# Optimization experiments

Measured on AMD Instinct MI355X. Metric: run time of the kernel, lower is better.

The kernel has to match this reference:

```python
import jax, jax.numpy as jnp
import numpy as np

B, L, M, C = 32, 688, 4, 32  # batch, otsl_sequence_length (= layout_prompt_length), max targets per box, tag vocab


def setup_inputs() -> dict:
    key = jax.random.key(0)
    ks = jax.random.split(key, 8)
    tag_logits = jax.random.normal(ks[0], (B, L, C), jnp.float32)
    pointer_logits = jax.random.normal(ks[1], (B, L, L), jnp.float32)
    empty_pointer_logits = jax.random.normal(ks[2], (B, 1, L), jnp.float32)
    tag_targets = jax.random.randint(ks[3], (B, L), 0, C)
    box = jax.random.randint(ks[4], (B, L, M), 0, L)
    keep = jax.random.bernoulli(ks[5], 0.5, (B, L, M))
    box_indices = jnp.where(keep, box, -1)  # -1 = padded / invalid target
    data_tag_mask = jax.random.bernoulli(ks[6], 0.3, (B, 2 * L))
    attention_mask = jax.random.bernoulli(ks[7], 0.8, (B, 2 * L)) | data_tag_mask
    return {
        'tag_logits': tag_logits,
        'pointer_logits': pointer_logits,
        'empty_pointer_logits': empty_pointer_logits,
        'tag_targets': tag_targets,
        'box_indices': box_indices,
        'data_tag_mask': data_tag_mask,
        'attention_mask': attention_mask,
    }


def reference(tag_logits, pointer_logits, empty_pointer_logits,
              tag_targets, box_indices, data_tag_mask, attention_mask):
    Bq, Lq, Cq = tag_logits.shape

    # ---- tag (cls) loss: mean cross-entropy over B*S positions ----
    logp = jax.nn.log_softmax(tag_logits, axis=-1)
    cls_loss = -jnp.mean(jnp.take_along_axis(logp, tag_targets[..., None], axis=-1))

    # ---- pointer loss: masked softmax over sequence positions ----
    seq_mask = data_tag_mask[:, Lq:]                                  # (B, L)
    mx = jnp.max(pointer_logits, axis=-1, keepdims=True)              # unmasked max, as in torch code
    exp_l = jnp.exp(pointer_logits - mx)                              # (B, L, L)
    denom = jnp.sum(exp_l * seq_mask[:, None, :], axis=-1, keepdims=True) + 1e-10
    # scatter target_mask[b, i, box_indices[b, i, m]] = True for valid entries
    valid = box_indices != -1                                         # (B, L, M)
    tgt = jnp.clip(box_indices, 0, Lq - 1)
    b_ix = jnp.arange(Bq)[:, None, None]
    r_ix = jnp.arange(Lq)[None, :, None]
    target_mask = jnp.zeros((Bq, Lq, Lq), bool).at[b_ix, r_ix, tgt].max(valid)
    losses = -jnp.log(exp_l / denom + 1e-10)                          # (B, L, L)
    masked = losses * (target_mask & seq_mask[:, None, :])
    cnt = jnp.sum(masked != 0)
    ptr_loss = jnp.where(cnt == 0, 0.0, jnp.sum(masked) / jnp.maximum(cnt, 1))

    # ---- empty pointer loss: BCE-with-logits, mean over attended positions ----
    seq2 = attention_mask[:, Lq:]                                     # (B, L)
    data2 = data_tag_mask[:, Lq:]
    targets = (seq2 & ~data2).astype(jnp.float32)
    x = empty_pointer_logits[:, 0, :]                                 # (B, L)
    bce = jnp.maximum(x, 0.0) - x * targets + jnp.log1p(jnp.exp(-jnp.abs(x)))
    vm = seq2.astype(jnp.float32)
    empty_ptr_loss = jnp.sum(bce * vm) / jnp.maximum(jnp.sum(vm), 1.0)

    # forward() returns early: total = cls + ptr + empty (no lambdas, contrastive dead code)
    total = cls_loss + ptr_loss + empty_ptr_loss
    return total, cls_loss, ptr_loss, empty_ptr_loss
```

## Files before the change

### kernel.cpp

```cpp
#include <hip/hip_runtime.h>
#include <hip/hip_bf16.h>
#include <math.h>

#define BB 32
#define LL 688
#define MM 4
#define CC 32
#define ROWS (BB * LL)
#define RPW 4
#define WPB 4
#define RPB (RPW * WPB)
#define NBLK (ROWS / RPB)

struct Partial { float4 a; float4 b; };

__device__ __forceinline__ float max12(float4 x, float4 y, float4 z) {
    return fmaxf(fmaxf(fmaxf(fmaxf(x.x, x.y), fmaxf(x.z, x.w)),
                       fmaxf(fmaxf(y.x, y.y), fmaxf(y.z, y.w))),
                 fmaxf(fmaxf(z.x, z.y), fmaxf(z.z, z.w)));
}

__device__ __forceinline__ float msum12(float4 x, float4 y, float4 z,
                                        float4 f0, float4 f1, float4 f2, float m) {
    float s = 0.f;
    s = fmaf(f0.x, __expf(x.x - m), s);
    s = fmaf(f0.y, __expf(x.y - m), s);
    s = fmaf(f0.z, __expf(x.z - m), s);
    s = fmaf(f0.w, __expf(x.w - m), s);
    s = fmaf(f1.x, __expf(y.x - m), s);
    s = fmaf(f1.y, __expf(y.y - m), s);
    s = fmaf(f1.z, __expf(y.z - m), s);
    s = fmaf(f1.w, __expf(y.w - m), s);
    s = fmaf(f2.x, __expf(z.x - m), s);
    s = fmaf(f2.y, __expf(z.y - m), s);
    s = fmaf(f2.z, __expf(z.z - m), s);
    s = fmaf(f2.w, __expf(z.w - m), s);
    return s;
}

__global__ __launch_bounds__(256) void fused_kernel(
    const float* __restrict__ tag_logits,
    const float* __restrict__ pl,
    const float* __restrict__ epl,
    const int* __restrict__ tag_targets,
    const int* __restrict__ box,
    const int* __restrict__ dtm,
    const int* __restrict__ am,
    Partial* __restrict__ partials)
{
    __shared__ float red[WPB][5];
    const int wave = threadIdx.x >> 6;
    const int lane = threadIdx.x & 63;
    const int row0 = blockIdx.x * RPB + wave * RPW;
    const int bat  = row0 / LL;
    const int jcol0 = row0 - bat * LL;

    const int* mrow = dtm + bat * (2 * LL) + LL;
    const int4* maskp = (const int4*)mrow;
    const bool has2 = (lane < 44);

    const int4 mi0 = maskp[lane];
    const int4 mi1 = maskp[lane + 64];
    const int4 mi2 = has2 ? maskp[lane + 128] : make_int4(0, 0, 0, 0);
    const float4 f0 = make_float4(mi0.x ? 1.f : 0.f, mi0.y ? 1.f : 0.f,
                                  mi0.z ? 1.f : 0.f, mi0.w ? 1.f : 0.f);
    const float4 f1 = make_float4(mi1.x ? 1.f : 0.f, mi1.y ? 1.f : 0.f,
                                  mi1.z ? 1.f : 0.f, mi1.w ? 1.f : 0.f);
    const float4 f2 = make_float4(mi2.x ? 1.f : 0.f, mi2.y ? 1.f : 0.f,
                                  mi2.z ? 1.f : 0.f, mi2.w ? 1.f : 0.f);

    const float4 NEGV = make_float4(-INFINITY, -INFINITY, -INFINITY, -INFINITY);
    const float4* rp0 = (const float4*)(pl + (size_t)(row0 + 0) * LL);
    const float4* rp1 = (const float4*)(pl + (size_t)(row0 + 1) * LL);
    const float4* rp2 = (const float4*)(pl + (size_t)(row0 + 2) * LL);
    const float4* rp3 = (const float4*)(pl + (size_t)(row0 + 3) * LL);

    const float4 a0 = rp0[lane], a1 = rp0[lane + 64], a2 = has2 ? rp0[lane + 128] : NEGV;
    const float4 c0 = rp1[lane], c1 = rp1[lane + 64], c2 = has2 ? rp1[lane + 128] : NEGV;
    const float4 d0 = rp2[lane], d1 = rp2[lane + 64], d2 = has2 ? rp2[lane + 128] : NEGV;
    const float4 e0 = rp3[lane], e1 = rp3[lane + 64], e2 = has2 ? rp3[lane + 128] : NEGV;

    float pm0 = max12(a0, a1, a2);
    float pm1 = max12(c0, c1, c2);
    float pm2 = max12(d0, d1, d2);
    float pm3 = max12(e0, e1, e2);
    #pragma unroll
    for (int off = 32; off >= 1; off >>= 1) {
        pm0 = fmaxf(pm0, __shfl_xor(pm0, off));
        pm1 = fmaxf(pm1, __shfl_xor(pm1, off));
        pm2 = fmaxf(pm2, __shfl_xor(pm2, off));
        pm3 = fmaxf(pm3, __shfl_xor(pm3, off));
    }

    float ps0 = msum12(a0, a1, a2, f0, f1, f2, pm0);
    float ps1 = msum12(c0, c1, c2, f0, f1, f2, pm1);
    float ps2 = msum12(d0, d1, d2, f0, f1, f2, pm2);
    float ps3 = msum12(e0, e1, e2, f0, f1, f2, pm3);
    #pragma unroll
    for (int off = 32; off >= 1; off >>= 1) {
        ps0 += __shfl_xor(ps0, off);
        ps1 += __shfl_xor(ps1, off);
        ps2 += __shfl_xor(ps2, off);
        ps3 += __shfl_xor(ps3, off);
    }

    const int rl  = lane & 15;
    const int r   = rl >> 2;
    const int mi  = rl & 3;
    const int rowr = row0 + r;
    const float mxr = (r == 0) ? pm0 : (r == 1) ? pm1 : (r == 2) ? pm2 : pm3;
    const float dnr = ((r == 0) ? ps0 : (r == 1) ? ps1 : (r == 2) ? ps2 : ps3) + 1e-10f;

    const int t = box[(size_t)rowr * MM + mi];
    const int ta  = __shfl(t, (lane & ~3));
    const int tb  = __shfl(t, (lane & ~3) + 1);
    const int tc2 = __shfl(t, (lane & ~3) + 2);
    const bool dup = (mi > 0 && t == ta) || (mi > 1 && t == tb) || (mi > 2 && t == tc2);
    const bool valid = (t >= 0);
    const int tcl = t < 0 ? 0 : (t > LL - 1 ? LL - 1 : t);

    float contrib = 0.f, ccnt = 0.f;
    if (valid && !dup && mrow[tcl]) {
        const float xj = pl[(size_t)rowr * LL + tcl];
        const float p = __expf(xj - mxr) / dnr + 1e-10f;
        const float v = -__logf(p);
        contrib = v;
        ccnt = (v != 0.0f) ? 1.f : 0.f;
    }
    contrib += __shfl_xor(contrib, 1); contrib += __shfl_xor(contrib, 2);
    ccnt    += __shfl_xor(ccnt, 1);    ccnt    += __shfl_xor(ccnt, 2);
    const float ptr_sum = __shfl(contrib, 0) + __shfl(contrib, 4) +
                          __shfl(contrib, 8) + __shfl(contrib, 12);
    const float ptr_cnt = __shfl(ccnt, 0) + __shfl(ccnt, 4) +
                          __shfl(ccnt, 8) + __shfl(ccnt, 12);

    float cls_tot = 0.f;
    #pragma unroll
    for (int pass = 0; pass < 2; ++pass) {
        const int rowc = row0 + pass * 2 + (lane >> 5);
        const float x = tag_logits[(size_t)rowc * CC + (lane & 31)];
        float cm = x;
        #pragma unroll
        for (int off = 16; off >= 1; off >>= 1)
            cm = fmaxf(cm, __shfl_xor(cm, off, 32));
        float cs = __expf(x - cm);
        #pragma unroll
        for (int off = 16; off >= 1; off >>= 1)
            cs += __shfl_xor(cs, off, 32);
        const int tg = tag_targets[rowc];
        const float xt = __shfl(x, tg + (lane & 32));
        const float c = (cm + __logf(cs)) - xt;
        cls_tot += __shfl(c, 0) + __shfl(c, 32);
    }

    const int rb = lane & 3;
    const int rowb = row0 + rb;
    const int offb = bat * (2 * LL) + LL + (jcol0 + rb);
    const int seq2  = am[offb];
    const int data2 = dtm[offb];
    const float xe = epl[rowb];
    const float te = (seq2 && !data2) ? 1.f : 0.f;
    const float bce = fmaxf(xe, 0.f) - xe * te + log1pf(__expf(-fabsf(xe)));
    float bsum = seq2 ? bce : 0.f;
    float vsum = seq2 ? 1.f : 0.f;
    bsum += __shfl_xor(bsum, 1); bsum += __shfl_xor(bsum, 2);
    vsum += __shfl_xor(vsum, 1); vsum += __shfl_xor(vsum, 2);

    if (lane == 0) {
        red[wave][0] = cls_tot;
        red[wave][1] = ptr_sum;
        red[wave][2] = ptr_cnt;
        red[wave][3] = bsum;
        red[wave][4] = vsum;
    }
    __syncthreads();
    if (threadIdx.x == 0) {
        Partial p;
        p.a.x = red[0][0] + red[1][0] + red[2][0] + red[3][0];
        p.a.y = red[0][1] + red[1][1] + red[2][1] + red[3][1];
        p.a.z = red[0][2] + red[1][2] + red[2][2] + red[3][2];
        p.a.w = red[0][3] + red[1][3] + red[2][3] + red[3][3];
        p.b = make_float4(red[0][4] + red[1][4] + red[2][4] + red[3][4], 0.f, 0.f, 0.f);
        partials[blockIdx.x] = p;
    }
}

__global__ __launch_bounds__(256) void reduce_kernel(const Partial* __restrict__ partials,
                                                     float* __restrict__ out)
{
    __shared__ float sm[4][5];
    float c = 0.f, p = 0.f, n = 0.f, e = 0.f, v = 0.f;
    for (int i = threadIdx.x; i < NBLK; i += 256) {
        const Partial q = partials[i];
        c += q.a.x; p += q.a.y; n += q.a.z; e += q.a.w; v += q.b.x;
    }
    #pragma unroll
    for (int off = 32; off >= 1; off >>= 1) {
        c += __shfl_xor(c, off);
        p += __shfl_xor(p, off);
        n += __shfl_xor(n, off);
        e += __shfl_xor(e, off);
        v += __shfl_xor(v, off);
    }
    const int wv = threadIdx.x >> 6;
    if ((threadIdx.x & 63) == 0) {
        sm[wv][0] = c; sm[wv][1] = p; sm[wv][2] = n; sm[wv][3] = e; sm[wv][4] = v;
    }
    __syncthreads();
    if (threadIdx.x == 0) {
        float tc = 0.f, tp = 0.f, tn = 0.f, tb = 0.f, tv = 0.f;
        #pragma unroll
        for (int i = 0; i < 4; ++i) {
            tc += sm[i][0]; tp += sm[i][1]; tn += sm[i][2];
            tb += sm[i][3]; tv += sm[i][4];
        }
        const float cls_loss = tc / (float)ROWS;
        const float ptr_loss = (tn == 0.f) ? 0.f : tp / fmaxf(tn, 1.f);
        const float emp_loss = tb / fmaxf(tv, 1.f);
        out[0] = cls_loss + ptr_loss + emp_loss;
        out[1] = cls_loss;
        out[2] = ptr_loss;
        out[3] = emp_loss;
    }
}

extern "C" void kernel_launch(void* const* d_in, const int* in_sizes, int n_in,
                              void* d_out, int out_size, void* d_ws, size_t ws_size,
                              hipStream_t stream) {
    const float* tag_logits           = (const float*)d_in[0];
    const float* pointer_logits       = (const float*)d_in[1];
    const float* empty_pointer_logits = (const float*)d_in[2];
    const int*   tag_targets          = (const int*)d_in[3];
    const int*   box_indices          = (const int*)d_in[4];
    const int*   data_tag_mask        = (const int*)d_in[5];
    const int*   attention_mask       = (const int*)d_in[6];
    float* out = (float*)d_out;
    Partial* partials = (Partial*)d_ws;

    fused_kernel<<<NBLK, 256, 0, stream>>>(tag_logits, pointer_logits,
                                           empty_pointer_logits, tag_targets,
                                           box_indices, data_tag_mask,
                                           attention_mask, partials);
    reduce_kernel<<<1, 256, 0, stream>>>(partials, out);
}
```

Before: 108.5 us.

## Fuse final reduction via last-block atomic counter and hoist all loads early

The separate reduce kernel is replaced by a last-block-done pattern: each block stores its partials, fences, and bumps an atomic counter, and the final block reduces all partials and writes the outputs. A memset of the counter is added to the launch sequence. All global loads (box targets, gathered pointer logit, tag logits, targets, BCE inputs) are hoisted before the softmax math and restricted to the lanes that need them, to overlap their latency with the main row loads. This trades one kernel launch for a memset plus an atomic and fences per block, and slightly higher register pressure.

```diff
diff --git a/kernel.cpp b/kernel.cpp
--- a/kernel.cpp
+++ b/kernel.cpp
@@ -11,8 +11,9 @@
 #define WPB 4
 #define RPB (RPW * WPB)
 #define NBLK (ROWS / RPB)
-
-struct Partial { float4 a; float4 b; };
+#define COUNTER_OFF 65536
+
+struct Partial { float v[8]; };
 
 __device__ __forceinline__ float max12(float4 x, float4 y, float4 z) {
     return fmaxf(fmaxf(fmaxf(fmaxf(x.x, x.y), fmaxf(x.z, x.w)),
@@ -46,9 +47,12 @@
     const int* __restrict__ box,
     const int* __restrict__ dtm,
     const int* __restrict__ am,
-    Partial* __restrict__ partials)
+    Partial* __restrict__ partials,
+    unsigned int* __restrict__ counter,
+    float* __restrict__ out)
 {
     __shared__ float red[WPB][5];
+    __shared__ int lastflag;
     const int wave = threadIdx.x >> 6;
     const int lane = threadIdx.x & 63;
     const int row0 = blockIdx.x * RPB + wave * RPW;
@@ -62,23 +66,51 @@
     const int4 mi0 = maskp[lane];
     const int4 mi1 = maskp[lane + 64];
     const int4 mi2 = has2 ? maskp[lane + 128] : make_int4(0, 0, 0, 0);
+
+    const float4 NEGV = make_float4(-INFINITY, -INFINITY, -INFINITY, -INFINITY);
+    const float4* rp0 = (const float4*)(pl + (size_t)(row0 + 0) * LL);
+    const float4* rp1 = (const float4*)(pl + (size_t)(row0 + 1) * LL);
+    const float4* rp2 = (const float4*)(pl + (size_t)(row0 + 2) * LL);
+    const float4* rp3 = (const float4*)(pl + (size_t)(row0 + 3) * LL);
+    const float4 a0 = rp0[lane], a1 = rp0[lane + 64], a2 = has2 ? rp0[lane + 128] : NEGV;
+    const float4 c0 = rp1[lane], c1 = rp1[lane + 64], c2 = has2 ? rp1[lane + 128] : NEGV;
+    const float4 d0 = rp2[lane], d1 = rp2[lane + 64], d2 = has2 ? rp2[lane + 128] : NEGV;
+    const float4 e0 = rp3[lane], e1 = rp3[lane + 64], e2 = has2 ? rp3[lane + 128] : NEGV;
+
+    const int r  = (lane & 15) >> 2;
+    const int mi = lane & 3;
+    const int rowr = row0 + r;
+    int t = -1, tmask = 0;
+    float xj = 0.f;
+    if (lane < 16) {
+        t = box[(size_t)rowr * MM + mi];
+        const int tcl = t < 0 ? 0 : (t > LL - 1 ? LL - 1 : t);
+        tmask = mrow[tcl];
+        xj = pl[(size_t)rowr * LL + tcl];
+    }
+
+    const int half = lane >> 5;
+    const int cid  = lane & 31;
+    const float clsx0 = tag_logits[(size_t)(row0 + half) * CC + cid];
+    const float clsx1 = tag_logits[(size_t)(row0 + 2 + half) * CC + cid];
+    const int tg0 = tag_targets[row0 + half];
+    const int tg1 = tag_targets[row0 + 2 + half];
+
+    int seq2 = 0, data2 = 0;
+    float xe = 0.f;
+    if (lane < 4) {
+        const int offb = bat * (2 * LL) + LL + (jcol0 + lane);
+        seq2  = am[offb];
+        data2 = dtm[offb];
+        xe    = epl[row0 + lane];
+    }
+
     const float4 f0 = make_float4(mi0.x ? 1.f : 0.f, mi0.y ? 1.f : 0.f,
                                   mi0.z ? 1.f : 0.f, mi0.w ? 1.f : 0.f);
     const float4 f1 = make_float4(mi1.x ? 1.f : 0.f, mi1.y ? 1.f : 0.f,
                                   mi1.z ? 1.f : 0.f, mi1.w ? 1.f : 0.f);
     const float4 f2 = make_float4(mi2.x ? 1.f : 0.f, mi2.y ? 1.f : 0.f,
                                   mi2.z ? 1.f : 0.f, mi2.w ? 1.f : 0.f);
-
-    const float4 NEGV = make_float4(-INFINITY, -INFINITY, -INFINITY, -INFINITY);
-    const float4* rp0 = (const float4*)(pl + (size_t)(row0 + 0) * LL);
-    const float4* rp1 = (const float4*)(pl + (size_t)(row0 + 1) * LL);
-    const float4* rp2 = (const float4*)(pl + (size_t)(row0 + 2) * LL);
-    const float4* rp3 = (const float4*)(pl + (size_t)(row0 + 3) * LL);
-
-    const float4 a0 = rp0[lane], a1 = rp0[lane + 64], a2 = has2 ? rp0[lane + 128] : NEGV;
-    const float4 c0 = rp1[lane], c1 = rp1[lane + 64], c2 = has2 ? rp1[lane + 128] : NEGV;
-    const float4 d0 = rp2[lane], d1 = rp2[lane + 64], d2 = has2 ? rp2[lane + 128] : NEGV;
-    const float4 e0 = rp3[lane], e1 = rp3[lane + 64], e2 = has2 ? rp3[lane + 128] : NEGV;
 
     float pm0 = max12(a0, a1, a2);
     float pm1 = max12(c0, c1, c2);
@@ -91,7 +123,6 @@
         pm2 = fmaxf(pm2, __shfl_xor(pm2, off));
         pm3 = fmaxf(pm3, __shfl_xor(pm3, off));
     }
-
     float ps0 = msum12(a0, a1, a2, f0, f1, f2, pm0);
     float ps1 = msum12(c0, c1, c2, f0, f1, f2, pm1);
     float ps2 = msum12(d0, d1, d2, f0, f1, f2, pm2);
@@ -104,28 +135,20 @@
         ps3 += __shfl_xor(ps3, off);
     }
 
-    const int rl  = lane & 15;
-    const int r   = rl >> 2;
-    const int mi  = rl & 3;
-    const int rowr = row0 + r;
-    const float mxr = (r == 0) ? pm0 : (r == 1) ? pm1 : (r == 2) ? pm2 : pm3;
-    const float dnr = ((r == 0) ? ps0 : (r == 1) ? ps1 : (r == 2) ? ps2 : ps3) + 1e-10f;
-
-    const int t = box[(size_t)rowr * MM + mi];
     const int ta  = __shfl(t, (lane & ~3));
     const int tb  = __shfl(t, (lane & ~3) + 1);
     const int tc2 = __shfl(t, (lane & ~3) + 2);
-    const bool dup = (mi > 0 && t == ta) || (mi > 1 && t == tb) || (mi > 2 && t == tc2);
-    const bool valid = (t >= 0);
-    const int tcl = t < 0 ? 0 : (t > LL - 1 ? LL - 1 : t);
-
     float contrib = 0.f, ccnt = 0.f;
-    if (valid && !dup && mrow[tcl]) {
-        const float xj = pl[(size_t)rowr * LL + tcl];
-        const float p = __expf(xj - mxr) / dnr + 1e-10f;
-        const float v = -__logf(p);
-        contrib = v;
-        ccnt = (v != 0.0f) ? 1.f : 0.f;
+    if (lane < 16) {
+        const bool dup = (mi > 0 && t == ta) || (mi > 1 && t == tb) || (mi > 2 && t == tc2);
+        if (t >= 0 && !dup && tmask) {
+            const float mxr = (r == 0) ? pm0 : (r == 1) ? pm1 : (r == 2) ? pm2 : pm3;
+            const float dnr = ((r == 0) ? ps0 : (r == 1) ? ps1 : (r == 2) ? ps2 : ps3) + 1e-10f;
+            const float p = __expf(xj - mxr) / dnr + 1e-10f;
+            const float v = -__logf(p);
+            contrib = v;
+            ccnt = (v != 0.0f) ? 1.f : 0.f;
+        }
     }
     contrib += __shfl_xor(contrib, 1); contrib += __shfl_xor(contrib, 2);
     ccnt    += __shfl_xor(ccnt, 1);    ccnt    += __shfl_xor(ccnt, 2);
@@ -135,34 +158,39 @@
                           __shfl(ccnt, 8) + __shfl(ccnt, 12);
 
     float cls_tot = 0.f;
-    #pragma unroll
-    for (int pass = 0; pass < 2; ++pass) {
-        const int rowc = row0 + pass * 2 + (lane >> 5);
-        const float x = tag_logits[(size_t)rowc * CC + (lane & 31)];
-        float cm = x;
+    {
+        float cm = clsx0;
         #pragma unroll
         for (int off = 16; off >= 1; off >>= 1)
             cm = fmaxf(cm, __shfl_xor(cm, off, 32));
-        float cs = __expf(x - cm);
+        float cs = __expf(clsx0 - cm);
         #pragma unroll
         for (int off = 16; off >= 1; off >>= 1)
             cs += __shfl_xor(cs, off, 32);
-        const int tg = tag_targets[rowc];
-        const float xt = __shfl(x, tg + (lane & 32));
+        const float xt = __shfl(clsx0, tg0 + (lane & 32));
         const float c = (cm + __logf(cs)) - xt;
         cls_tot += __shfl(c, 0) + __shfl(c, 32);
     }
-
-    const int rb = lane & 3;
-    const int rowb = row0 + rb;
-    const int offb = bat * (2 * LL) + LL + (jcol0 + rb);
-    const int seq2  = am[offb];
-    const int data2 = dtm[offb];
-    const float xe = epl[rowb];
-    const float te = (seq2 && !data2) ? 1.f : 0.f;
-    const float bce = fmaxf(xe, 0.f) - xe * te + log1pf(__expf(-fabsf(xe)));
-    float bsum = seq2 ? bce : 0.f;
-    float vsum = seq2 ? 1.f : 0.f;
+    {
+        float cm = clsx1;
+        #pragma unroll
+        for (int off = 16; off >= 1; off >>= 1)
+            cm = fmaxf(cm, __shfl_xor(cm, off, 32));
+        float cs = __expf(clsx1 - cm);
+        #pragma unroll
+        for (int off = 16; off >= 1; off >>= 1)
+            cs += __shfl_xor(cs, off, 32);
+        const float xt = __shfl(clsx1, tg1 + (lane & 32));
+        const float c = (cm + __logf(cs)) - xt;
+        cls_tot += __shfl(c, 0) + __shfl(c, 32);
+    }
+
+    float bsum = 0.f, vsum = 0.f;
+    if (lane < 4 && seq2) {
+        const float te = (!data2) ? 1.f : 0.f;
+        bsum = fmaxf(xe, 0.f) - xe * te + log1pf(__expf(-fabsf(xe)));
+        vsum = 1.f;
+    }
     bsum += __shfl_xor(bsum, 1); bsum += __shfl_xor(bsum, 2);
     vsum += __shfl_xor(vsum, 1); vsum += __shfl_xor(vsum, 2);
 
@@ -175,52 +203,62 @@
     }
     __syncthreads();
     if (threadIdx.x == 0) {
-        Partial p;
-        p.a.x = red[0][0] + red[1][0] + red[2][0] + red[3][0];
-        p.a.y = red[0][1] + red[1][1] + red[2][1] + red[3][1];
-        p.a.z = red[0][2] + red[1][2] + red[2][2] + red[3][2];
-        p.a.w = red[0][3] + red[1][3] + red[2][3] + red[3][3];
-        p.b = make_float4(red[0][4] + red[1][4] + red[2][4] + red[3][4], 0.f, 0.f, 0.f);
-        partials[blockIdx.x] = p;
-    }
-}
-
-__global__ __launch_bounds__(256) void reduce_kernel(const Partial* __restrict__ partials,
-                                                     float* __restrict__ out)
-{
-    __shared__ float sm[4][5];
-    float c = 0.f, p = 0.f, n = 0.f, e = 0.f, v = 0.f;
-    for (int i = threadIdx.x; i < NBLK; i += 256) {
-        const Partial q = partials[i];
-        c += q.a.x; p += q.a.y; n += q.a.z; e += q.a.w; v += q.b.x;
-    }
-    #pragma unroll
-    for (int off = 32; off >= 1; off >>= 1) {
-        c += __shfl_xor(c, off);
-        p += __shfl_xor(p, off);
-        n += __shfl_xor(n, off);
-        e += __shfl_xor(e, off);
-        v += __shfl_xor(v, off);
-    }
-    const int wv = threadIdx.x >> 6;
-    if ((threadIdx.x & 63) == 0) {
-        sm[wv][0] = c; sm[wv][1] = p; sm[wv][2] = n; sm[wv][3] = e; sm[wv][4] = v;
+        float p0 = red[0][0] + red[1][0] + red[2][0] + red[3][0];
+        float p1 = red[0][1] + red[1][1] + red[2][1] + red[3][1];
+        float p2 = red[0][2] + red[1][2] + red[2][2] + red[3][2];
+        float p3 = red[0][3] + red[1][3] + red[2][3] + red[3][3];
+        float p4 = red[0][4] + red[1][4] + red[2][4] + red[3][4];
+        float* q = partials[blockIdx.x].v;
+        __hip_atomic_store(q + 0, p0, __ATOMIC_RELAXED, __HIP_MEMORY_SCOPE_AGENT);
+        __hip_atomic_store(q + 1, p1, __ATOMIC_RELAXED, __HIP_MEMORY_SCOPE_AGENT);
+        __hip_atomic_store(q + 2, p2, __ATOMIC_RELAXED, __HIP_MEMORY_SCOPE_AGENT);
+        __hip_atomic_store(q + 3, p3, __ATOMIC_RELAXED, __HIP_MEMORY_SCOPE_AGENT);
+        __hip_atomic_store(q + 4, p4, __ATOMIC_RELAXED, __HIP_MEMORY_SCOPE_AGENT);
+        __threadfence();
+        const unsigned old = atomicAdd(counter, 1u);
+        lastflag = (old == NBLK - 1) ? 1 : 0;
     }
     __syncthreads();
-    if (threadIdx.x == 0) {
-        float tc = 0.f, tp = 0.f, tn = 0.f, tb = 0.f, tv = 0.f;
-        #pragma unroll
-        for (int i = 0; i < 4; ++i) {
-            tc += sm[i][0]; tp += sm[i][1]; tn += sm[i][2];
-            tb += sm[i][3]; tv += sm[i][4];
-        }
-        const float cls_loss = tc / (float)ROWS;
-        const float ptr_loss = (tn == 0.f) ? 0.f : tp / fmaxf(tn, 1.f);
-        const float emp_loss = tb / fmaxf(tv, 1.f);
-        out[0] = cls_loss + ptr_loss + emp_loss;
-        out[1] = cls_loss;
-        out[2] = ptr_loss;
-        out[3] = emp_loss;
+
+    if (lastflag) {
+        __threadfence();
+        float c = 0.f, p = 0.f, n = 0.f, e = 0.f, v = 0.f;
+        for (int i = threadIdx.x; i < NBLK; i += 256) {
+            const float* q = partials[i].v;
+            c += __hip_atomic_load(q + 0, __ATOMIC_RELAXED, __HIP_MEMORY_SCOPE_AGENT);
+            p += __hip_atomic_load(q + 1, __ATOMIC_RELAXED, __HIP_MEMORY_SCOPE_AGENT);
+            n += __hip_atomic_load(q + 2, __ATOMIC_RELAXED, __HIP_MEMORY_SCOPE_AGENT);
+            e += __hip_atomic_load(q + 3, __ATOMIC_RELAXED, __HIP_MEMORY_SCOPE_AGENT);
+            v += __hip_atomic_load(q + 4, __ATOMIC_RELAXED, __HIP_MEMORY_SCOPE_AGENT);
+        }
+        #pragma unroll
+        for (int off = 32; off >= 1; off >>= 1) {
+            c += __shfl_xor(c, off);
+            p += __shfl_xor(p, off);
+            n += __shfl_xor(n, off);
+            e += __shfl_xor(e, off);
+            v += __shfl_xor(v, off);
+        }
+        if (lane == 0) {
+            red[wave][0] = c; red[wave][1] = p; red[wave][2] = n;
+            red[wave][3] = e; red[wave][4] = v;
+        }
+        __syncthreads();
+        if (threadIdx.x == 0) {
+            float tc = 0.f, tp = 0.f, tn = 0.f, tb = 0.f, tv = 0.f;
+            #pragma unroll
+            for (int i = 0; i < WPB; ++i) {
+                tc += red[i][0]; tp += red[i][1]; tn += red[i][2];
+                tb += red[i][3]; tv += red[i][4];
+            }
+            const float cls_loss = tc / (float)ROWS;
+            const float ptr_loss = (tn == 0.f) ? 0.f : tp / fmaxf(tn, 1.f);
+            const float emp_loss = tb / fmaxf(tv, 1.f);
+            out[0] = cls_loss + ptr_loss + emp_loss;
+            out[1] = cls_loss;
+            out[2] = ptr_loss;
+            out[3] = emp_loss;
+        }
     }
 }
 
@@ -236,10 +274,11 @@
     const int*   attention_mask       = (const int*)d_in[6];
     float* out = (float*)d_out;
     Partial* partials = (Partial*)d_ws;
-
+    unsigned int* counter = (unsigned int*)((char*)d_ws + COUNTER_OFF);
+
+    hipMemsetAsync(counter, 0, sizeof(unsigned int), stream);
     fused_kernel<<<NBLK, 256, 0, stream>>>(tag_logits, pointer_logits,
                                            empty_pointer_logits, tag_targets,
                                            box_indices, data_tag_mask,
-                                           attention_mask, partials);
-    reduce_kernel<<<1, 256, 0, stream>>>(partials, out);
-}
+                                           attention_mask, partials, counter, out);
+}
```

Result: slower. 147.4 us (+35.8%).

## Use single-wave blocks with two rows per wave and hoist all loads early

Applied to the files above, without the earlier changes.

The fused kernel now runs one 64-thread wave per block, each handling two rows instead of four, which removes the shared-memory block reduction and __syncthreads and doubles the number of partials. All global loads (pointer rows, box targets, gathered logit, tag logits, empty-pointer inputs) are issued up front, before any reductions, to raise memory-level parallelism. The final reduce kernel grows to 1024 threads to absorb the larger partial count. The cost is a much larger grid of tiny blocks, more partial-sum traffic, and a heavier single-block final reduction.

```diff
diff --git a/kernel.cpp b/kernel.cpp
--- a/kernel.cpp
+++ b/kernel.cpp
@@ -7,12 +7,10 @@
 #define MM 4
 #define CC 32
 #define ROWS (BB * LL)
-#define RPW 4
-#define WPB 4
-#define RPB (RPW * WPB)
-#define NBLK (ROWS / RPB)
-
-struct Partial { float4 a; float4 b; };
+#define RPW 2
+#define NPART (ROWS / RPW)
+
+struct Partial { float v[8]; };
 
 __device__ __forceinline__ float max12(float4 x, float4 y, float4 z) {
     return fmaxf(fmaxf(fmaxf(fmaxf(x.x, x.y), fmaxf(x.z, x.w)),
@@ -38,7 +36,7 @@
     return s;
 }
 
-__global__ __launch_bounds__(256) void fused_kernel(
+__global__ __launch_bounds__(64) void fused_kernel(
     const float* __restrict__ tag_logits,
     const float* __restrict__ pl,
     const float* __restrict__ epl,
@@ -48,10 +46,8 @@
     const int* __restrict__ am,
     Partial* __restrict__ partials)
 {
-    __shared__ float red[WPB][5];
-    const int wave = threadIdx.x >> 6;
-    const int lane = threadIdx.x & 63;
-    const int row0 = blockIdx.x * RPB + wave * RPW;
+    const int lane = threadIdx.x;
+    const int row0 = blockIdx.x * RPW;
     const int bat  = row0 / LL;
     const int jcol0 = row0 - bat * LL;
 
@@ -62,6 +58,39 @@
     const int4 mi0 = maskp[lane];
     const int4 mi1 = maskp[lane + 64];
     const int4 mi2 = has2 ? maskp[lane + 128] : make_int4(0, 0, 0, 0);
+
+    const float4 NEGV = make_float4(-INFINITY, -INFINITY, -INFINITY, -INFINITY);
+    const float4* rp0 = (const float4*)(pl + (size_t)(row0 + 0) * LL);
+    const float4* rp1 = (const float4*)(pl + (size_t)(row0 + 1) * LL);
+    const float4 a0 = rp0[lane], a1 = rp0[lane + 64], a2 = has2 ? rp0[lane + 128] : NEGV;
+    const float4 c0 = rp1[lane], c1 = rp1[lane + 64], c2 = has2 ? rp1[lane + 128] : NEGV;
+
+    const int r  = (lane & 7) >> 2;
+    const int mi = lane & 3;
+    const int rowr = row0 + r;
+    int t = -1, tmask = 0;
+    float xj = 0.f;
+    if (lane < 8) {
+        t = box[(size_t)rowr * MM + mi];
+        const int tcl = t < 0 ? 0 : (t > LL - 1 ? LL - 1 : t);
+        tmask = mrow[tcl];
+        xj = pl[(size_t)rowr * LL + tcl];
+    }
+
+    const int half = lane >> 5;
+    const int cid  = lane & 31;
+    const float clsx = tag_logits[(size_t)(row0 + half) * CC + cid];
+    const int   tg   = tag_targets[row0 + half];
+
+    int seq2 = 0, data2 = 0;
+    float xe = 0.f;
+    if (lane < 2) {
+        const int offb = bat * (2 * LL) + LL + (jcol0 + lane);
+        seq2  = am[offb];
+        data2 = dtm[offb];
+        xe    = epl[row0 + lane];
+    }
+
     const float4 f0 = make_float4(mi0.x ? 1.f : 0.f, mi0.y ? 1.f : 0.f,
                                   mi0.z ? 1.f : 0.f, mi0.w ? 1.f : 0.f);
     const float4 f1 = make_float4(mi1.x ? 1.f : 0.f, mi1.y ? 1.f : 0.f,
@@ -69,130 +98,78 @@
     const float4 f2 = make_float4(mi2.x ? 1.f : 0.f, mi2.y ? 1.f : 0.f,
                                   mi2.z ? 1.f : 0.f, mi2.w ? 1.f : 0.f);
 
-    const float4 NEGV = make_float4(-INFINITY, -INFINITY, -INFINITY, -INFINITY);
-    const float4* rp0 = (const float4*)(pl + (size_t)(row0 + 0) * LL);
-    const float4* rp1 = (const float4*)(pl + (size_t)(row0 + 1) * LL);
-    const float4* rp2 = (const float4*)(pl + (size_t)(row0 + 2) * LL);
-    const float4* rp3 = (const float4*)(pl + (size_t)(row0 + 3) * LL);
-
-    const float4 a0 = rp0[lane], a1 = rp0[lane + 64], a2 = has2 ? rp0[lane + 128] : NEGV;
-    const float4 c0 = rp1[lane], c1 = rp1[lane + 64], c2 = has2 ? rp1[lane + 128] : NEGV;
-    const float4 d0 = rp2[lane], d1 = rp2[lane + 64], d2 = has2 ? rp2[lane + 128] : NEGV;
-    const float4 e0 = rp3[lane], e1 = rp3[lane + 64], e2 = has2 ? rp3[lane + 128] : NEGV;
-
     float pm0 = max12(a0, a1, a2);
     float pm1 = max12(c0, c1, c2);
-    float pm2 = max12(d0, d1, d2);
-    float pm3 = max12(e0, e1, e2);
     #pragma unroll
     for (int off = 32; off >= 1; off >>= 1) {
         pm0 = fmaxf(pm0, __shfl_xor(pm0, off));
         pm1 = fmaxf(pm1, __shfl_xor(pm1, off));
-        pm2 = fmaxf(pm2, __shfl_xor(pm2, off));
-        pm3 = fmaxf(pm3, __shfl_xor(pm3, off));
-    }
-
+    }
     float ps0 = msum12(a0, a1, a2, f0, f1, f2, pm0);
     float ps1 = msum12(c0, c1, c2, f0, f1, f2, pm1);
-    float ps2 = msum12(d0, d1, d2, f0, f1, f2, pm2);
-    float ps3 = msum12(e0, e1, e2, f0, f1, f2, pm3);
     #pragma unroll
     for (int off = 32; off >= 1; off >>= 1) {
         ps0 += __shfl_xor(ps0, off);
         ps1 += __shfl_xor(ps1, off);
-        ps2 += __shfl_xor(ps2, off);
-        ps3 += __shfl_xor(ps3, off);
-    }
-
-    const int rl  = lane & 15;
-    const int r   = rl >> 2;
-    const int mi  = rl & 3;
-    const int rowr = row0 + r;
-    const float mxr = (r == 0) ? pm0 : (r == 1) ? pm1 : (r == 2) ? pm2 : pm3;
-    const float dnr = ((r == 0) ? ps0 : (r == 1) ? ps1 : (r == 2) ? ps2 : ps3) + 1e-10f;
-
-    const int t = box[(size_t)rowr * MM + mi];
+    }
+
     const int ta  = __shfl(t, (lane & ~3));
     const int tb  = __shfl(t, (lane & ~3) + 1);
     const int tc2 = __shfl(t, (lane & ~3) + 2);
-    const bool dup = (mi > 0 && t == ta) || (mi > 1 && t == tb) || (mi > 2 && t == tc2);
-    const bool valid = (t >= 0);
-    const int tcl = t < 0 ? 0 : (t > LL - 1 ? LL - 1 : t);
-
     float contrib = 0.f, ccnt = 0.f;
-    if (valid && !dup && mrow[tcl]) {
-        const float xj = pl[(size_t)rowr * LL + tcl];
-        const float p = __expf(xj - mxr) / dnr + 1e-10f;
-        const float v = -__logf(p);
-        contrib = v;
-        ccnt = (v != 0.0f) ? 1.f : 0.f;
+    if (lane < 8) {
+        const bool dup = (mi > 0 && t == ta) || (mi > 1 && t == tb) || (mi > 2 && t == tc2);
+        if (t >= 0 && !dup && tmask) {
+            const float mxr = (r == 0) ? pm0 : pm1;
+            const float dnr = ((r == 0) ? ps0 : ps1) + 1e-10f;
+            const float p = __expf(xj - mxr) / dnr + 1e-10f;
+            const float v = -__logf(p);
+            contrib = v;
+            ccnt = (v != 0.0f) ? 1.f : 0.f;
+        }
     }
     contrib += __shfl_xor(contrib, 1); contrib += __shfl_xor(contrib, 2);
     ccnt    += __shfl_xor(ccnt, 1);    ccnt    += __shfl_xor(ccnt, 2);
-    const float ptr_sum = __shfl(contrib, 0) + __shfl(contrib, 4) +
-                          __shfl(contrib, 8) + __shfl(contrib, 12);
-    const float ptr_cnt = __shfl(ccnt, 0) + __shfl(ccnt, 4) +
-                          __shfl(ccnt, 8) + __shfl(ccnt, 12);
-
-    float cls_tot = 0.f;
-    #pragma unroll
-    for (int pass = 0; pass < 2; ++pass) {
-        const int rowc = row0 + pass * 2 + (lane >> 5);
-        const float x = tag_logits[(size_t)rowc * CC + (lane & 31)];
-        float cm = x;
-        #pragma unroll
-        for (int off = 16; off >= 1; off >>= 1)
-            cm = fmaxf(cm, __shfl_xor(cm, off, 32));
-        float cs = __expf(x - cm);
-        #pragma unroll
-        for (int off = 16; off >= 1; off >>= 1)
-            cs += __shfl_xor(cs, off, 32);
-        const int tg = tag_targets[rowc];
-        const float xt = __shfl(x, tg + (lane & 32));
-        const float c = (cm + __logf(cs)) - xt;
-        cls_tot += __shfl(c, 0) + __shfl(c, 32);
-    }
-
-    const int rb = lane & 3;
-    const int rowb = row0 + rb;
-    const int offb = bat * (2 * LL) + LL + (jcol0 + rb);
-    const int seq2  = am[offb];
-    const int data2 = dtm[offb];
-    const float xe = epl[rowb];
-    const float te = (seq2 && !data2) ? 1.f : 0.f;
-    const float bce = fmaxf(xe, 0.f) - xe * te + log1pf(__expf(-fabsf(xe)));
-    float bsum = seq2 ? bce : 0.f;
-    float vsum = seq2 ? 1.f : 0.f;
-    bsum += __shfl_xor(bsum, 1); bsum += __shfl_xor(bsum, 2);
-    vsum += __shfl_xor(vsum, 1); vsum += __shfl_xor(vsum, 2);
+    const float ptr_sum = __shfl(contrib, 0) + __shfl(contrib, 4);
+    const float ptr_cnt = __shfl(ccnt, 0) + __shfl(ccnt, 4);
+
+    float cm = clsx;
+    #pragma unroll
+    for (int off = 16; off >= 1; off >>= 1)
+        cm = fmaxf(cm, __shfl_xor(cm, off, 32));
+    float cs = __expf(clsx - cm);
+    #pragma unroll
+    for (int off = 16; off >= 1; off >>= 1)
+        cs += __shfl_xor(cs, off, 32);
+    const float xt = __shfl(clsx, tg + (lane & 32));
+    const float c = (cm + __logf(cs)) - xt;
+    const float cls_tot = __shfl(c, 0) + __shfl(c, 32);
+
+    float bsum = 0.f, vsum = 0.f;
+    if (lane < 2 && seq2) {
+        const float te = (!data2) ? 1.f : 0.f;
+        bsum = fmaxf(xe, 0.f) - xe * te + log1pf(__expf(-fabsf(xe)));
+        vsum = 1.f;
+    }
+    bsum += __shfl_xor(bsum, 1);
+    vsum += __shfl_xor(vsum, 1);
 
     if (lane == 0) {
-        red[wave][0] = cls_tot;
-        red[wave][1] = ptr_sum;
-        red[wave][2] = ptr_cnt;
-        red[wave][3] = bsum;
-        red[wave][4] = vsum;
-    }
-    __syncthreads();
-    if (threadIdx.x == 0) {
-        Partial p;
-        p.a.x = red[0][0] + red[1][0] + red[2][0] + red[3][0];
-        p.a.y = red[0][1] + red[1][1] + red[2][1] + red[3][1];
-        p.a.z = red[0][2] + red[1][2] + red[2][2] + red[3][2];
-        p.a.w = red[0][3] + red[1][3] + red[2][3] + red[3][3];
-        p.b = make_float4(red[0][4] + red[1][4] + red[2][4] + red[3][4], 0.f, 0.f, 0.f);
-        partials[blockIdx.x] = p;
-    }
-}
-
-__global__ __launch_bounds__(256) void reduce_kernel(const Partial* __restrict__ partials,
-                                                     float* __restrict__ out)
+        float* q = partials[blockIdx.x].v;
+        *(float4*)q = make_float4(cls_tot, ptr_sum, ptr_cnt, bsum);
+        q[4] = vsum;
+    }
+}
+
+__global__ __launch_bounds__(1024) void reduce_kernel(const Partial* __restrict__ partials,
+                                                      float* __restrict__ out)
 {
-    __shared__ float sm[4][5];
+    __shared__ float sm[16][5];
     float c = 0.f, p = 0.f, n = 0.f, e = 0.f, v = 0.f;
-    for (int i = threadIdx.x; i < NBLK; i += 256) {
-        const Partial q = partials[i];
-        c += q.a.x; p += q.a.y; n += q.a.z; e += q.a.w; v += q.b.x;
+    for (int i = threadIdx.x; i < NPART; i += 1024) {
+        const float* q = partials[i].v;
+        const float4 a = *(const float4*)q;
+        c += a.x; p += a.y; n += a.z; e += a.w; v += q[4];
     }
     #pragma unroll
     for (int off = 32; off >= 1; off >>= 1) {
@@ -210,7 +187,7 @@
     if (threadIdx.x == 0) {
         float tc = 0.f, tp = 0.f, tn = 0.f, tb = 0.f, tv = 0.f;
         #pragma unroll
-        for (int i = 0; i < 4; ++i) {
+        for (int i = 0; i < 16; ++i) {
             tc += sm[i][0]; tp += sm[i][1]; tn += sm[i][2];
             tb += sm[i][3]; tv += sm[i][4];
         }
@@ -237,9 +214,9 @@
     float* out = (float*)d_out;
     Partial* partials = (Partial*)d_ws;
 
-    fused_kernel<<<NBLK, 256, 0, stream>>>(tag_logits, pointer_logits,
+    fused_kernel<<<NPART, 64, 0, stream>>>(tag_logits, pointer_logits,
                                            empty_pointer_logits, tag_targets,
                                            box_indices, data_tag_mask,
                                            attention_mask, partials);
-    reduce_kernel<<<1, 256, 0, stream>>>(partials, out);
-}
+    reduce_kernel<<<1, 1024, 0, stream>>>(partials, out);
+}
```

Measured after the change: 114.0 us. 1.05x slower.
